# Performance work log

Hardware: AMD Instinct MI355X
Metric: run time of the kernel (lower is better)

Reference implementation:

```python
import jax, jax.numpy as jnp
import numpy as np

N, E, L = 50000, 800000, 3
EPS = 1e-5


def mlp2(h, W1, b1, W2, b2):
    # Linear -> ReLU -> Linear
    return jax.nn.relu(h @ W1 + b1) @ W2 + b2


def setup_inputs() -> dict:
    key = jax.random.key(0)
    ks = jax.random.split(key, 20)
    s = 0.1  # weight scale to keep activations well-conditioned
    return {
        "x": jax.random.normal(ks[0], (N, 128), jnp.float32),
        "edge_attr": jax.random.normal(ks[1], (E, 64), jnp.float32),
        "edge_index": jax.random.randint(ks[2], (2, E), 0, N, dtype=jnp.int32),
        "Wn1": jax.random.normal(ks[3], (L, 128, 256), jnp.float32) * s,
        "bn1": jnp.zeros((L, 256), jnp.float32),
        "Wn2": jax.random.normal(ks[4], (L, 256, 128), jnp.float32) * s,
        "bn2": jnp.zeros((L, 128), jnp.float32),
        "We1": jax.random.normal(ks[5], (L, 64, 128), jnp.float32) * s,
        "be1": jnp.zeros((L, 128), jnp.float32),
        "We2": jax.random.normal(ks[6], (L, 128, 64), jnp.float32) * s,
        "be2": jnp.zeros((L, 64), jnp.float32),
        "Wm1": jax.random.normal(ks[7], (L, 320, 128), jnp.float32) * s,
        "bm1": jnp.zeros((L, 128), jnp.float32),
        "Wm2": jax.random.normal(ks[8], (L, 128, 128), jnp.float32) * s,
        "bm2": jnp.zeros((L, 128), jnp.float32),
        "lnw": jnp.ones((L, 128), jnp.float32),
        "lnb": jnp.zeros((L, 128), jnp.float32),
        "Wf": jax.random.normal(ks[9], (128, 64), jnp.float32) * s,
        "bf": jnp.zeros((64,), jnp.float32),
    }


def reference(x, edge_attr, edge_index, Wn1, bn1, Wn2, bn2, We1, be1, We2, be2,
              Wm1, bm1, Wm2, bm2, lnw, lnb, Wf, bf):
    src, dst = edge_index[0], edge_index[1]  # x_j = x[src], x_i = x[dst] (PyG source_to_target)
    deg = jax.ops.segment_sum(jnp.ones((E,), x.dtype), dst, num_segments=N)
    denom = jnp.maximum(deg, 1.0)[:, None]  # scatter-mean with clamp for isolated nodes
    for l in range(L):
        # mlp_node is the same function for x_i and x_j -> apply once per node, then gather
        xn = mlp2(x, Wn1[l], bn1[l], Wn2[l], bn2[l])        # [N, 128]
        e = mlp2(edge_attr, We1[l], be1[l], We2[l], be2[l])  # [E, 64]
        m = jnp.concatenate([xn[dst], xn[src], e], axis=-1)  # [E, 320] = [x_i, x_j, edge_attr]
        m = mlp2(m, Wm1[l], bm1[l], Wm2[l], bm2[l])          # [E, 128]
        agg = jax.ops.segment_sum(m, dst, num_segments=N) / denom  # mean aggregate [N, 128]
        mu = agg.mean(-1, keepdims=True)
        var = agg.var(-1, keepdims=True)
        h = (agg - mu) * jax.lax.rsqrt(var + EPS) * lnw[l] + lnb[l]  # LayerNorm
        x = jax.nn.relu(h)  # dropout p=0.0 -> identity
    return x @ Wf + bf  # jk='last' -> final linear on last layer output
```

## Files before the change

### kernel.cpp

```cpp
#include <hip/hip_runtime.h>
#include <stdint.h>

#define NN 50000
#define NE 800000
#define NB 196

typedef float f32x4 __attribute__((ext_vector_type(4)));
typedef short bf16x8 __attribute__((ext_vector_type(8)));

__device__ __forceinline__ unsigned short f2bf(float f) {
  union { float f; unsigned u; } v; v.f = f;
  unsigned r = v.u + 0x7fffu + ((v.u >> 16) & 1u);
  return (unsigned short)(r >> 16);
}
__device__ __forceinline__ float bf2f(unsigned short h) {
  union { unsigned u; float f; } v; v.u = ((unsigned)h) << 16;
  return v.f;
}
__device__ __forceinline__ float ldf(const void* p, size_t i, int m32) {
  return m32 ? ((const float*)p)[i] : bf2f(((const unsigned short*)p)[i]);
}

__global__ void detect_kernel(const void* lnw, int* flag) {
  if (threadIdx.x == 0 && blockIdx.x == 0)
    *flag = (((const unsigned short*)lnw)[0] == 0x3F80) ? 0 : 1;
}

#define oWn1 0
#define oWn2 98304
#define oWm1 196608
#define oWe1 319488
#define oWe2 344064
#define oWm2 368640
#define oWf  417792
#define NWTOT 425984
#define obn1 0
#define obn2 768
#define obe1 1152
#define obe2 1536
#define obm1 1728
#define obm2 2112
#define olnw 2496
#define olnb 2880
#define obf  3264
#define NBTOT 3328

__global__ __launch_bounds__(256) void conv_w(
    const void* Wn1, const void* Wn2, const void* Wm1, const void* We1,
    const void* We2, const void* Wm2, const void* Wf,
    const int* __restrict__ flg, unsigned short* __restrict__ cW)
{
  const int m32 = *flg;
  int i = blockIdx.x * 256 + threadIdx.x;
  if (i >= NWTOT) return;
  const void* src; size_t j;
  if      (i < oWn2) { src = Wn1; j = i - oWn1; }
  else if (i < oWm1) { src = Wn2; j = i - oWn2; }
  else if (i < oWe1) { src = Wm1; j = i - oWm1; }
  else if (i < oWe2) { src = We1; j = i - oWe1; }
  else if (i < oWm2) { src = We2; j = i - oWe2; }
  else if (i < oWf)  { src = Wm2; j = i - oWm2; }
  else               { src = Wf;  j = i - oWf;  }
  cW[i] = f2bf(ldf(src, j, m32));
}

__global__ __launch_bounds__(256) void conv_b(
    const void* bn1, const void* bn2, const void* be1, const void* be2,
    const void* bm1, const void* bm2, const void* lnw, const void* lnb,
    const void* bfv, const int* __restrict__ flg, float* __restrict__ cB)
{
  const int m32 = *flg;
  int i = blockIdx.x * 256 + threadIdx.x;
  if (i >= NBTOT) return;
  const void* src; size_t j;
  if      (i < obn2) { src = bn1; j = i - obn1; }
  else if (i < obe1) { src = bn2; j = i - obn2; }
  else if (i < obe2) { src = be1; j = i - obe1; }
  else if (i < obm1) { src = be2; j = i - obe2; }
  else if (i < obm2) { src = bm1; j = i - obm1; }
  else if (i < olnw) { src = bm2; j = i - obm2; }
  else if (i < olnb) { src = lnw; j = i - olnw; }
  else if (i < obf)  { src = lnb; j = i - olnb; }
  else               { src = bfv; j = i - obf;  }
  cB[i] = ldf(src, j, m32);
}

__global__ __launch_bounds__(256) void conv_x(const void* x, const int* flg,
                                              unsigned short* xc) {
  const int m32 = *flg;
  size_t i = (size_t)blockIdx.x * 256 + threadIdx.x;
  if (i < (size_t)NN * 128) xc[i] = f2bf(ldf(x, i, m32));
}

__global__ __launch_bounds__(256) void deg_int(const int* __restrict__ eidx,
                                               int* __restrict__ degi) {
  int i = blockIdx.x * 256 + threadIdx.x;
  if (i < NE) atomicAdd(degi + eidx[NE + i], 1);
}

__global__ __launch_bounds__(256) void scan1(const int* __restrict__ degi,
                                             int* __restrict__ base,
                                             int* __restrict__ bsum) {
  __shared__ int s[256];
  int t = threadIdx.x, i = blockIdx.x * 256 + t;
  int v = (i < NN) ? degi[i] : 0;
  s[t] = v; __syncthreads();
  for (int d = 1; d < 256; d <<= 1) {
    int u = (t >= d) ? s[t - d] : 0;
    __syncthreads();
    s[t] += u;
    __syncthreads();
  }
  if (i < NN) base[i] = s[t] - v;
  if (t == 255) bsum[blockIdx.x] = s[255];
}

__global__ void scan2(int* bsum) {
  __shared__ int s[256];
  int t = threadIdx.x;
  int v = (t < NB) ? bsum[t] : 0;
  s[t] = v; __syncthreads();
  for (int d = 1; d < 256; d <<= 1) {
    int u = (t >= d) ? s[t - d] : 0;
    __syncthreads();
    s[t] += u;
    __syncthreads();
  }
  if (t < NB) bsum[t] = s[t] - v;
}

__global__ __launch_bounds__(256) void scan3(int* base, const int* bsum) {
  int i = blockIdx.x * 256 + threadIdx.x;
  if (i < NN) base[i] += bsum[blockIdx.x];
}

__global__ __launch_bounds__(256) void scatter_sort(
    const int* __restrict__ eidx, const int* __restrict__ base,
    int* __restrict__ cursor, int* __restrict__ sE) {
  int e = blockIdx.x * 256 + threadIdx.x;
  if (e < NE) {
    int d = eidx[NE + e];
    int r = atomicAdd(cursor + d, 1);
    sE[base[d] + r] = e;
  }
}

__global__ __launch_bounds__(256) void prep_wc(
    const unsigned short* __restrict__ cW, const float* __restrict__ cB,
    float* __restrict__ Wc, float* __restrict__ bc2)
{
  int l = blockIdx.x;
  const unsigned short* We2l = cW + oWe2 + l * 8192;
  const unsigned short* Wm1c = cW + oWm1 + l * 40960 + 256 * 128;
  const float* be2l = cB + obe2 + l * 64;
  const float* bm1l = cB + obm1 + l * 128;
  float* out = Wc + l * 16384;
  for (int i = threadIdx.x; i < 16384; i += 256) {
    int k = i >> 7, n = i & 127;
    float s = 0.f;
    for (int u = 0; u < 64; u++)
      s += bf2f(We2l[k * 64 + u]) * bf2f(Wm1c[u * 128 + n]);
    out[i] = s;
  }
  if (threadIdx.x < 128) {
    int n = threadIdx.x;
    float s = bm1l[n];
    for (int u = 0; u < 64; u++)
      s += bf2f(be2l[u]) * bf2f(Wm1c[u * 128 + n]);
    bc2[l * 128 + n] = s;
  }
}

__global__ __launch_bounds__(256) void pack_frags(
    const unsigned short* __restrict__ cW, const float* __restrict__ Wcp,
    unsigned short* __restrict__ Wn1p, unsigned short* __restrict__ Wn2p,
    unsigned short* __restrict__ Wm1p, unsigned short* __restrict__ We1p,
    unsigned short* __restrict__ Wcpk)
{
  int l = blockIdx.x / 5, which = blockIdx.x % 5;
  int K, N, total;
  const unsigned short* src = nullptr;
  const float* srcf = nullptr;
  unsigned short* dst;
  if (which == 0)      { K = 128; N = 256; src = cW + oWn1 + (size_t)l * 32768; dst = Wn1p + (size_t)l * 32768; }
  else if (which == 1) { K = 256; N = 128; src = cW + oWn2 + (size_t)l * 32768; dst = Wn2p + (size_t)l * 32768; }
  else if (which == 2) { K = 128; N = 256; src = cW + oWm1 + (size_t)l * 40960; dst = Wm1p + (size_t)l * 32768; }
  else if (which == 3) { K = 64;  N = 128; src = cW + oWe1 + (size_t)l * 8192;  dst = We1p + (size_t)l * 8192; }
  else                 { K = 128; N = 128; srcf = Wcp + (size_t)l * 16384;      dst = Wcpk + (size_t)l * 16384; }
  int KB = K >> 5;
  total = K * N;
  for (int o = threadIdx.x; o < total; o += 256) {
    int j = o & 7, lane = (o >> 3) & 63, q = o >> 9;
    int kb = q % KB, c = q / KB;
    int k = kb * 32 + (lane >> 4) * 8 + j;
    int n = c * 16 + (lane & 15);
    unsigned short v;
    if (which == 2) {
      v = (n < 128) ? src[k * 128 + n] : src[(128 + k) * 128 + (n - 128)];
    } else if (which == 4) {
      v = f2bf(srcf[k * 128 + n]);
    } else {
      v = src[k * N + n];
    }
    dst[o] = v;
  }
}

__global__ __launch_bounds__(256) void node_p_mfma(
    const unsigned short* __restrict__ xin,
    const unsigned short* __restrict__ Wn1p, const unsigned short* __restrict__ Wn2p,
    const unsigned short* __restrict__ Wm1p, const float* __restrict__ cB,
    unsigned short* __restrict__ P, int l)
{
  __shared__ __align__(16) short HS[4][16 * 256];
  const int tid = threadIdx.x;
  const int wid = tid >> 6, lane = tid & 63, rl = lane & 15, cg = lane >> 4;
  const int n0 = blockIdx.x * 64;
  short* Hw = &HS[wid][0];
  const int swr = (rl & 7) << 3;

  int nA = n0 + wid * 16 + rl;
  int nAc = (nA < NN) ? nA : (NN - 1);

  bf16x8 ax[4];
  {
    const unsigned short* xr = xin + (size_t)nAc * 128;
    #pragma unroll
    for (int kb = 0; kb < 4; kb++)
      ax[kb] = *(const bf16x8*)&xr[kb * 32 + cg * 8];
  }

  {
    const unsigned short* Wb = Wn1p + (size_t)l * 32768;
    const float* b1 = cB + obn1 + l * 256;
    #pragma unroll
    for (int c = 0; c < 16; c++) {
      f32x4 acc = {0.f, 0.f, 0.f, 0.f};
      #pragma unroll
      for (int kb = 0; kb < 4; kb++) {
        bf16x8 b = *(const bf16x8*)&Wb[(size_t)(c * 4 + kb) * 512 + lane * 8];
        acc = __builtin_amdgcn_mfma_f32_16x16x32_bf16(ax[kb], b, acc, 0, 0, 0);
      }
      int col = c * 16 + rl;
      float bb = b1[col];
      #pragma unroll
      for (int r = 0; r < 4; r++) {
        int row = cg * 4 + r;
        Hw[row * 256 + (col ^ ((row & 7) << 3))] =
            (short)f2bf(fmaxf(acc[r] + bb, 0.f));
      }
    }
  }

  {
    bf16x8 ah[8];
    #pragma unroll
    for (int kb = 0; kb < 8; kb++)
      ah[kb] = *(const bf16x8*)&Hw[rl * 256 + ((kb * 32 + cg * 8) ^ swr)];
    const unsigned short* Wb = Wn2p + (size_t)l * 32768;
    const float* b2 = cB + obn2 + l * 128;
    #pragma unroll
    for (int c = 0; c < 8; c++) {
      f32x4 acc = {0.f, 0.f, 0.f, 0.f};
      #pragma unroll
      for (int kb = 0; kb < 8; kb++) {
        bf16x8 b = *(const bf16x8*)&Wb[(size_t)(c * 8 + kb) * 512 + lane * 8];
        acc = __builtin_amdgcn_mfma_f32_16x16x32_bf16(ah[kb], b, acc, 0, 0, 0);
      }
      int col = c * 16 + rl;
      float bb = b2[col];
      #pragma unroll
      for (int r = 0; r < 4; r++) {
        int row = cg * 4 + r;
        Hw[row * 128 + (col ^ ((row & 7) << 3))] = (short)f2bf(acc[r] + bb);
      }
    }
  }

  {
    bf16x8 an[4];
    #pragma unroll
    for (int kb = 0; kb < 4; kb++)
      an[kb] = *(const bf16x8*)&Hw[rl * 128 + ((kb * 32 + cg * 8) ^ swr)];
    const unsigned short* Wb = Wm1p + (size_t)l * 32768;
    #pragma unroll
    for (int c = 0; c < 16; c++) {
      f32x4 acc = {0.f, 0.f, 0.f, 0.f};
      #pragma unroll
      for (int kb = 0; kb < 4; kb++) {
        bf16x8 b = *(const bf16x8*)&Wb[(size_t)(c * 4 + kb) * 512 + lane * 8];
        acc = __builtin_amdgcn_mfma_f32_16x16x32_bf16(an[kb], b, acc, 0, 0, 0);
      }
      int col = c * 16 + rl;
      #pragma unroll
      for (int r = 0; r < 4; r++) {
        int row = cg * 4 + r;
        int n = n0 + wid * 16 + row;
        if (n < NN) P[(size_t)n * 256 + col] = f2bf(acc[r]);
      }
    }
  }
}

__global__ __launch_bounds__(256) void edge_fold_mfma(
    const void* __restrict__ ea, const int* __restrict__ eidx,
    const int* __restrict__ sE,
    const unsigned short* __restrict__ We1p, const unsigned short* __restrict__ Wcpk,
    const float* __restrict__ cB, const float* __restrict__ bc2,
    const unsigned short* __restrict__ P, unsigned short* __restrict__ Hb,
    const int* __restrict__ flg, int l)
{
  __shared__ __align__(16) short r1S[4][16 * 128];
  const int m32 = *flg;
  const int tid = threadIdx.x;
  const int wid = tid >> 6, lane = tid & 63, rl = lane & 15, cg = lane >> 4;
  const int e0 = blockIdx.x * 64;
  short* Rw = &r1S[wid][0];
  const int swr = (rl & 7) << 3;

  int eidA = sE[e0 + wid * 16 + rl];
  bf16x8 a0, a1;
  if (m32) {
    const float* er = (const float*)ea + (size_t)eidA * 64;
    f32x4 u0 = *(const f32x4*)&er[cg * 8];
    f32x4 u1 = *(const f32x4*)&er[cg * 8 + 4];
    f32x4 u2 = *(const f32x4*)&er[32 + cg * 8];
    f32x4 u3 = *(const f32x4*)&er[32 + cg * 8 + 4];
    alignas(16) unsigned short t0[8], t1[8];
    #pragma unroll
    for (int j = 0; j < 4; j++) {
      t0[j] = f2bf(u0[j]); t0[4 + j] = f2bf(u1[j]);
      t1[j] = f2bf(u2[j]); t1[4 + j] = f2bf(u3[j]);
    }
    a0 = *(const bf16x8*)t0; a1 = *(const bf16x8*)t1;
  } else {
    const unsigned short* er = (const unsigned short*)ea + (size_t)eidA * 64;
    a0 = *(const bf16x8*)&er[cg * 8];
    a1 = *(const bf16x8*)&er[32 + cg * 8];
  }

  {
    const unsigned short* Wb = We1p + (size_t)l * 8192;
    const float* be1l = cB + obe1 + l * 128;
    #pragma unroll
    for (int c = 0; c < 8; c++) {
      bf16x8 b0 = *(const bf16x8*)&Wb[(c * 2 + 0) * 512 + lane * 8];
      bf16x8 b1 = *(const bf16x8*)&Wb[(c * 2 + 1) * 512 + lane * 8];
      f32x4 acc = {0.f, 0.f, 0.f, 0.f};
      acc = __builtin_amdgcn_mfma_f32_16x16x32_bf16(a0, b0, acc, 0, 0, 0);
      acc = __builtin_amdgcn_mfma_f32_16x16x32_bf16(a1, b1, acc, 0, 0, 0);
      int col = c * 16 + rl;
      float b = be1l[col];
      #pragma unroll
      for (int r = 0; r < 4; r++) {
        int row = cg * 4 + r;
        Rw[row * 128 + (col ^ ((row & 7) << 3))] =
            (short)f2bf(fmaxf(acc[r] + b, 0.f));
      }
    }
  }

  f32x4 acc2[8];
  {
    bf16x8 ra[4];
    #pragma unroll
    for (int kb = 0; kb < 4; kb++)
      ra[kb] = *(const bf16x8*)&Rw[rl * 128 + ((kb * 32 + cg * 8) ^ swr)];
    const unsigned short* Wb = Wcpk + (size_t)l * 16384;
    #pragma unroll
    for (int c = 0; c < 8; c++) {
      f32x4 acc = {0.f, 0.f, 0.f, 0.f};
      #pragma unroll
      for (int kb = 0; kb < 4; kb++) {
        bf16x8 b = *(const bf16x8*)&Wb[(c * 4 + kb) * 512 + lane * 8];
        acc = __builtin_amdgcn_mfma_f32_16x16x32_bf16(ra[kb], b, acc, 0, 0, 0);
      }
      acc2[c] = acc;
    }
  }

  const float* bc2l = bc2 + l * 128;
  #pragma unroll
  for (int r = 0; r < 4; r++) {
    int row = cg * 4 + r;
    int slot = e0 + wid * 16 + row;
    int eid = sE[slot];
    int si = eidx[eid], di = eidx[NE + eid];
    const unsigned short* Pd = P + (size_t)di * 256;
    const unsigned short* Ps = P + (size_t)si * 256 + 128;
    unsigned short* hrow = Hb + (size_t)slot * 128;
    #pragma unroll
    for (int c = 0; c < 8; c++) {
      int col = c * 16 + rl;
      float h = acc2[c][r] + bc2l[col] + bf2f(Pd[col]) + bf2f(Ps[col]);
      hrow[col] = f2bf(fmaxf(h, 0.f));
    }
  }
}

__global__ __launch_bounds__(256) void seg_agg_ln(
    const unsigned short* __restrict__ Hb, const int* __restrict__ base,
    const int* __restrict__ degi,
    const unsigned short* __restrict__ cW, const float* __restrict__ cB,
    unsigned short* __restrict__ xnext, int l)
{
  __shared__ float at[8][128];
  __shared__ float vs[8][128];
  const int tid = threadIdx.x;
  const int n0 = blockIdx.x * 8;
  {
    int g = tid >> 4;
    int j = g >> 1;
    int qp = g & 1;
    int c8 = (tid & 15) * 8;
    int n = n0 + j;
    int b0 = base[n], d = degi[n];
    float s[8] = {0.f, 0.f, 0.f, 0.f, 0.f, 0.f, 0.f, 0.f};
    for (int q = qp; q < d; q += 2) {
      bf16x8 v = *(const bf16x8*)&Hb[(size_t)(b0 + q) * 128 + c8];
      #pragma unroll
      for (int k = 0; k < 8; k++) s[k] += bf2f((unsigned short)v[k]);
    }
    float inv = 1.f / (float)(d > 0 ? d : 1);
    if (qp == 0) {
      #pragma unroll
      for (int k = 0; k < 8; k++) at[j][c8 + k] = s[k] * inv;
    }
    __syncthreads();
    if (qp == 1) {
      #pragma unroll
      for (int k = 0; k < 8; k++) at[j][c8 + k] += s[k] * inv;
    }
  }
  __syncthreads();
  {
    const int t = tid & 127, grp = tid >> 7;
    float acc[4] = {0.f, 0.f, 0.f, 0.f};
    const unsigned short* W = cW + oWm2 + (size_t)l * 16384 + t;
    for (int k = 0; k < 128; k += 4) {
      float w0 = bf2f(W[(k + 0) * 128]);
      float w1 = bf2f(W[(k + 1) * 128]);
      float w2 = bf2f(W[(k + 2) * 128]);
      float w3 = bf2f(W[(k + 3) * 128]);
      #pragma unroll
      for (int j = 0; j < 4; j++) {
        f32x4 v = *(const f32x4*)&at[grp * 4 + j][k];
        acc[j] += v[0] * w0 + v[1] * w1 + v[2] * w2 + v[3] * w3;
      }
    }
    float bm = cB[obm2 + l * 128 + t];
    #pragma unroll
    for (int j = 0; j < 4; j++) {
      int n = n0 + grp * 4 + j;
      vs[grp * 4 + j][t] = acc[j] + (degi[n] > 0 ? bm : 0.f);
    }
  }
  __syncthreads();
  const int w = tid >> 6, lane = tid & 63;
  float lw0 = cB[olnw + l * 128 + lane], lb0 = cB[olnb + l * 128 + lane];
  float lw1 = cB[olnw + l * 128 + lane + 64], lb1 = cB[olnb + l * 128 + lane + 64];
  #pragma unroll
  for (int jj = 0; jj < 2; jj++) {
    int j = w * 2 + jj;
    float v0 = vs[j][lane], v1 = vs[j][lane + 64];
    float s = v0 + v1, q = v0 * v0 + v1 * v1;
    #pragma unroll
    for (int m = 1; m < 64; m <<= 1) {
      s += __shfl_xor(s, m, 64);
      q += __shfl_xor(q, m, 64);
    }
    float mu = s * (1.f / 128.f);
    float var = fmaxf(q * (1.f / 128.f) - mu * mu, 0.f);
    float rs = rsqrtf(var + 1e-5f);
    int n = n0 + j;
    xnext[(size_t)n * 128 + lane] = f2bf(fmaxf((v0 - mu) * rs * lw0 + lb0, 0.f));
    xnext[(size_t)n * 128 + lane + 64] = f2bf(fmaxf((v1 - mu) * rs * lw1 + lb1, 0.f));
  }
}

__global__ __launch_bounds__(256) void final_k(
    const unsigned short* __restrict__ xc, const unsigned short* __restrict__ cW,
    const float* __restrict__ cB, const int* __restrict__ flg,
    void* __restrict__ out)
{
  const int m32 = *flg;
  const int tid = threadIdx.x;
  const int t = tid & 63;
  const int nd = blockIdx.x * 4 + (tid >> 6);
  float acc = cB[obf + t];
  const unsigned short* xr = xc + (size_t)nd * 128;
  const unsigned short* W = cW + oWf + t;
  for (int k = 0; k < 128; k++)
    acc += bf2f(xr[k]) * bf2f(W[(size_t)k * 64]);
  if (m32) ((float*)out)[(size_t)nd * 64 + t] = acc;
  else ((unsigned short*)out)[(size_t)nd * 64 + t] = f2bf(acc);
}

extern "C" void kernel_launch(void* const* d_in, const int* in_sizes, int n_in,
                              void* d_out, int out_size, void* d_ws, size_t ws_size,
                              hipStream_t stream) {
  (void)in_sizes; (void)n_in; (void)out_size; (void)ws_size;
  const void* x    = d_in[0];
  const void* ea   = d_in[1];
  const int*  eidx = (const int*)d_in[2];
  const void* Wn1  = d_in[3];
  const void* bn1  = d_in[4];
  const void* Wn2  = d_in[5];
  const void* bn2  = d_in[6];
  const void* We1  = d_in[7];
  const void* be1  = d_in[8];
  const void* We2  = d_in[9];
  const void* be2  = d_in[10];
  const void* Wm1  = d_in[11];
  const void* bm1  = d_in[12];
  const void* Wm2  = d_in[13];
  const void* bm2  = d_in[14];
  const void* lnw  = d_in[15];
  const void* lnb  = d_in[16];
  const void* Wf   = d_in[17];
  const void* bfv  = d_in[18];

  char* ws = (char*)d_ws;
  size_t off = 0;
  auto alloc = [&](size_t bytes) {
    size_t o = off;
    off += (bytes + 255) & ~(size_t)255;
    return o;
  };
  int*            flag = (int*)(ws + alloc(4));
  unsigned short* xcur = (unsigned short*)(ws + alloc((size_t)NN * 128 * 2));
  unsigned short* Pb   = (unsigned short*)(ws + alloc((size_t)NN * 256 * 2));
  unsigned short* cW   = (unsigned short*)(ws + alloc((size_t)NWTOT * 2));
  float*          cB   = (float*)(ws + alloc((size_t)NBTOT * 4));
  float*          Wcp  = (float*)(ws + alloc(3 * 16384 * 4));
  float*          bc2w = (float*)(ws + alloc(3 * 128 * 4));
  unsigned short* We1p = (unsigned short*)(ws + alloc(3 * 8192 * 2));
  unsigned short* Wcpk = (unsigned short*)(ws + alloc(3 * 16384 * 2));
  unsigned short* Wn1p = (unsigned short*)(ws + alloc(3 * 32768 * 2));
  unsigned short* Wn2p = (unsigned short*)(ws + alloc(3 * 32768 * 2));
  unsigned short* Wm1p = (unsigned short*)(ws + alloc(3 * 32768 * 2));
  int*            degi = (int*)(ws + alloc((size_t)NN * 4));
  int*            baseb= (int*)(ws + alloc((size_t)NN * 4));
  int*            bsum = (int*)(ws + alloc(256 * 4));
  int*            curs = (int*)(ws + alloc((size_t)NN * 4));
  int*            sE   = (int*)(ws + alloc((size_t)NE * 4));
  unsigned short* Hb   = (unsigned short*)(ws + alloc((size_t)NE * 128 * 2));

  detect_kernel<<<1, 64, 0, stream>>>(lnw, flag);
  conv_w<<<(NWTOT + 255) / 256, 256, 0, stream>>>(Wn1, Wn2, Wm1, We1, We2, Wm2,
                                                  Wf, flag, cW);
  conv_b<<<(NBTOT + 255) / 256, 256, 0, stream>>>(bn1, bn2, be1, be2, bm1, bm2,
                                                  lnw, lnb, bfv, flag, cB);
  conv_x<<<(NN * 128 + 255) / 256, 256, 0, stream>>>(x, flag, xcur);

  hipMemsetAsync(degi, 0, (size_t)NN * 4, stream);
  deg_int<<<(NE + 255) / 256, 256, 0, stream>>>(eidx, degi);
  scan1<<<NB, 256, 0, stream>>>(degi, baseb, bsum);
  scan2<<<1, 256, 0, stream>>>(bsum);
  scan3<<<NB, 256, 0, stream>>>(baseb, bsum);
  hipMemsetAsync(curs, 0, (size_t)NN * 4, stream);
  scatter_sort<<<(NE + 255) / 256, 256, 0, stream>>>(eidx, baseb, curs, sE);

  prep_wc<<<3, 256, 0, stream>>>(cW, cB, Wcp, bc2w);
  pack_frags<<<15, 256, 0, stream>>>(cW, Wcp, Wn1p, Wn2p, Wm1p, We1p, Wcpk);

  for (int l = 0; l < 3; l++) {
    node_p_mfma<<<(NN + 63) / 64, 256, 0, stream>>>(xcur, Wn1p, Wn2p, Wm1p,
                                                    cB, Pb, l);
    edge_fold_mfma<<<NE / 64, 256, 0, stream>>>(ea, eidx, sE, We1p, Wcpk, cB,
                                                bc2w, Pb, Hb, flag, l);
    seg_agg_ln<<<NN / 8, 256, 0, stream>>>(Hb, baseb, degi, cW, cB, xcur, l);
  }
  final_k<<<NN / 4, 256, 0, stream>>>(xcur, cW, cB, flag, d_out);
}
```

Baseline: 1.717 ms.

## Fuse segment aggregation into edge kernel via in-block segmented reduction and atomics

The edge kernel no longer writes the per-edge hidden activations (E×128 bf16) to global memory. It stages them in shared memory, applies the gathered node projections with vectorized loads, and does a segmented sum over the dst-sorted edges in the block. Fully contained segments are stored directly and boundary segments use float atomics into a zeroed N×128 fp32 buffer. This removes a large write plus re-read of the edge buffer, at the cost of a memset per layer, atomics, fp32 accumulation order changes, and a serial 64-iteration scan by half the threads.

```diff
diff --git a/kernel.cpp b/kernel.cpp
--- a/kernel.cpp
+++ b/kernel.cpp
@@ -302,23 +302,31 @@
   }
 }
 
-__global__ __launch_bounds__(256) void edge_fold_mfma(
+__global__ __launch_bounds__(256) void edge_fold_fused(
     const void* __restrict__ ea, const int* __restrict__ eidx,
-    const int* __restrict__ sE,
+    const int* __restrict__ sE, const int* __restrict__ baseg,
+    const int* __restrict__ degg,
     const unsigned short* __restrict__ We1p, const unsigned short* __restrict__ Wcpk,
     const float* __restrict__ cB, const float* __restrict__ bc2,
-    const unsigned short* __restrict__ P, unsigned short* __restrict__ Hb,
+    const unsigned short* __restrict__ P, float* __restrict__ agg,
     const int* __restrict__ flg, int l)
 {
-  __shared__ __align__(16) short r1S[4][16 * 128];
+  __shared__ __align__(16) char SB[64 * 132 * 4];
+  __shared__ int dstS[64], srcS[64];
+  float* hS = (float*)SB;
   const int m32 = *flg;
   const int tid = threadIdx.x;
   const int wid = tid >> 6, lane = tid & 63, rl = lane & 15, cg = lane >> 4;
   const int e0 = blockIdx.x * 64;
-  short* Rw = &r1S[wid][0];
+  short* Rw = (short*)(SB + wid * 4096);
   const int swr = (rl & 7) << 3;
 
-  int eidA = sE[e0 + wid * 16 + rl];
+  const int brow = wid * 16 + rl;
+  int eidA = sE[e0 + brow];
+  if (cg == 0) {
+    srcS[brow] = eidx[eidA];
+    dstS[brow] = eidx[NE + eidA];
+  }
   bf16x8 a0, a1;
   if (m32) {
     const float* er = (const float*)ea + (size_t)eidA * 64;
@@ -379,28 +387,74 @@
     }
   }
 
-  const float* bc2l = bc2 + l * 128;
+  __syncthreads();
+
   #pragma unroll
-  for (int r = 0; r < 4; r++) {
-    int row = cg * 4 + r;
-    int slot = e0 + wid * 16 + row;
-    int eid = sE[slot];
-    int si = eidx[eid], di = eidx[NE + eid];
-    const unsigned short* Pd = P + (size_t)di * 256;
-    const unsigned short* Ps = P + (size_t)si * 256 + 128;
-    unsigned short* hrow = Hb + (size_t)slot * 128;
-    #pragma unroll
-    for (int c = 0; c < 8; c++) {
-      int col = c * 16 + rl;
-      float h = acc2[c][r] + bc2l[col] + bf2f(Pd[col]) + bf2f(Ps[col]);
-      hrow[col] = f2bf(fmaxf(h, 0.f));
-    }
-  }
-}
-
-__global__ __launch_bounds__(256) void seg_agg_ln(
-    const unsigned short* __restrict__ Hb, const int* __restrict__ base,
-    const int* __restrict__ degi,
+  for (int c = 0; c < 8; c++) {
+    int col = c * 16 + rl;
+    #pragma unroll
+    for (int r = 0; r < 4; r++) {
+      int row = wid * 16 + cg * 4 + r;
+      hS[row * 132 + col] = acc2[c][r];
+    }
+  }
+  __syncthreads();
+
+  {
+    const int colg = tid & 15;
+    const int rc = tid >> 4;
+    const float* bc2l = bc2 + l * 128 + colg * 8;
+    float bcv[8];
+    #pragma unroll
+    for (int j = 0; j < 8; j++) bcv[j] = bc2l[j];
+    #pragma unroll
+    for (int rr = 0; rr < 4; rr++) {
+      int row = rc * 4 + rr;
+      int di = dstS[row], si = srcS[row];
+      float* hp = hS + row * 132 + colg * 8;
+      f32x4 h0 = *(const f32x4*)hp;
+      f32x4 h1 = *(const f32x4*)(hp + 4);
+      bf16x8 pd = *(const bf16x8*)(P + (size_t)di * 256 + colg * 8);
+      bf16x8 ps = *(const bf16x8*)(P + (size_t)si * 256 + 128 + colg * 8);
+      #pragma unroll
+      for (int j = 0; j < 4; j++) {
+        h0[j] = fmaxf(h0[j] + bcv[j] + bf2f((unsigned short)pd[j]) +
+                      bf2f((unsigned short)ps[j]), 0.f);
+        h1[j] = fmaxf(h1[j] + bcv[4 + j] + bf2f((unsigned short)pd[4 + j]) +
+                      bf2f((unsigned short)ps[4 + j]), 0.f);
+      }
+      *(f32x4*)hp = h0;
+      *(f32x4*)(hp + 4) = h1;
+    }
+  }
+  __syncthreads();
+
+  if (tid < 128) {
+    const int col = tid;
+    float run = 0.f;
+    int cur = dstS[0];
+    for (int i = 0; i < 64; i++) {
+      int d = dstS[i];
+      if (d != cur) {
+        int b0 = baseg[cur], dg = degg[cur];
+        if (b0 >= e0 && b0 + dg <= e0 + 64)
+          agg[(size_t)cur * 128 + col] = run;
+        else
+          atomicAdd(agg + (size_t)cur * 128 + col, run);
+        run = 0.f; cur = d;
+      }
+      run += hS[i * 132 + col];
+    }
+    int b0 = baseg[cur], dg = degg[cur];
+    if (b0 >= e0 && b0 + dg <= e0 + 64)
+      agg[(size_t)cur * 128 + col] = run;
+    else
+      atomicAdd(agg + (size_t)cur * 128 + col, run);
+  }
+}
+
+__global__ __launch_bounds__(256) void agg_w_ln(
+    const float* __restrict__ aggH, const int* __restrict__ degi,
     const unsigned short* __restrict__ cW, const float* __restrict__ cB,
     unsigned short* __restrict__ xnext, int l)
 {
@@ -408,29 +462,11 @@
   __shared__ float vs[8][128];
   const int tid = threadIdx.x;
   const int n0 = blockIdx.x * 8;
-  {
-    int g = tid >> 4;
-    int j = g >> 1;
-    int qp = g & 1;
-    int c8 = (tid & 15) * 8;
+  for (int i = tid; i < 1024; i += 256) {
+    int j = i >> 7, k = i & 127;
     int n = n0 + j;
-    int b0 = base[n], d = degi[n];
-    float s[8] = {0.f, 0.f, 0.f, 0.f, 0.f, 0.f, 0.f, 0.f};
-    for (int q = qp; q < d; q += 2) {
-      bf16x8 v = *(const bf16x8*)&Hb[(size_t)(b0 + q) * 128 + c8];
-      #pragma unroll
-      for (int k = 0; k < 8; k++) s[k] += bf2f((unsigned short)v[k]);
-    }
-    float inv = 1.f / (float)(d > 0 ? d : 1);
-    if (qp == 0) {
-      #pragma unroll
-      for (int k = 0; k < 8; k++) at[j][c8 + k] = s[k] * inv;
-    }
-    __syncthreads();
-    if (qp == 1) {
-      #pragma unroll
-      for (int k = 0; k < 8; k++) at[j][c8 + k] += s[k] * inv;
-    }
+    int d = degi[n];
+    at[j][k] = aggH[(size_t)n * 128 + k] / (float)(d > 0 ? d : 1);
   }
   __syncthreads();
   {
@@ -530,6 +566,7 @@
   int*            flag = (int*)(ws + alloc(4));
   unsigned short* xcur = (unsigned short*)(ws + alloc((size_t)NN * 128 * 2));
   unsigned short* Pb   = (unsigned short*)(ws + alloc((size_t)NN * 256 * 2));
+  float*          aggH = (float*)(ws + alloc((size_t)NN * 128 * 4));
   unsigned short* cW   = (unsigned short*)(ws + alloc((size_t)NWTOT * 2));
   float*          cB   = (float*)(ws + alloc((size_t)NBTOT * 4));
   float*          Wcp  = (float*)(ws + alloc(3 * 16384 * 4));
@@ -544,7 +581,6 @@
   int*            bsum = (int*)(ws + alloc(256 * 4));
   int*            curs = (int*)(ws + alloc((size_t)NN * 4));
   int*            sE   = (int*)(ws + alloc((size_t)NE * 4));
-  unsigned short* Hb   = (unsigned short*)(ws + alloc((size_t)NE * 128 * 2));
 
   detect_kernel<<<1, 64, 0, stream>>>(lnw, flag);
   conv_w<<<(NWTOT + 255) / 256, 256, 0, stream>>>(Wn1, Wn2, Wm1, We1, We2, Wm2,
@@ -567,9 +603,11 @@
   for (int l = 0; l < 3; l++) {
     node_p_mfma<<<(NN + 63) / 64, 256, 0, stream>>>(xcur, Wn1p, Wn2p, Wm1p,
                                                     cB, Pb, l);
-    edge_fold_mfma<<<NE / 64, 256, 0, stream>>>(ea, eidx, sE, We1p, Wcpk, cB,
-                                                bc2w, Pb, Hb, flag, l);
-    seg_agg_ln<<<NN / 8, 256, 0, stream>>>(Hb, baseb, degi, cW, cB, xcur, l);
+    hipMemsetAsync(aggH, 0, (size_t)NN * 128 * 4, stream);
+    edge_fold_fused<<<NE / 64, 256, 0, stream>>>(ea, eidx, sE, baseb, degi,
+                                                 We1p, Wcpk, cB, bc2w, Pb,
+                                                 aggH, flag, l);
+    agg_w_ln<<<NN / 8, 256, 0, stream>>>(aggH, degi, cW, cB, xcur, l);
   }
   final_k<<<NN / 4, 256, 0, stream>>>(xcur, cW, cB, flag, d_out);
 }
```

Result: faster. 1.591 ms (-7.4%).
